# Kernel tuning notes

Hardware: AMD Instinct MI355X
Metric: run time of the kernel (lower is better)

Reference implementation:

```python
import jax, jax.numpy as jnp
import numpy as np

P = 8        # num policies
Z = 64       # per-policy latent dim
D = P * Z    # total latent dim = 512
A = 8        # action dim
H = 512      # hidden dim
B = 8192     # batch


def setup_inputs() -> dict:
    key = jax.random.key(0)
    ks = jax.random.split(key, 10)
    IN = Z + A
    s1 = 1.0 / np.sqrt(IN)
    s2 = 1.0 / np.sqrt(H)
    return {
        "latents": jax.random.normal(ks[0], (B, D), dtype=jnp.float32),
        "actions": jax.random.normal(ks[1], (B, A), dtype=jnp.float32),
        "policy_indices": jax.random.randint(ks[2], (B,), 0, P, dtype=jnp.int64) if jax.config.jax_enable_x64 else jax.random.randint(ks[2], (B,), 0, P, dtype=jnp.int32),
        # Stacked params for P_outer x P_inner MLPs: (z+A) -> H -> H -> Z
        "W1": jax.random.uniform(ks[3], (P, P, IN, H), jnp.float32, -s1, s1),
        "b1": jax.random.uniform(ks[4], (P, P, H), jnp.float32, -s1, s1),
        "W2": jax.random.uniform(ks[5], (P, P, H, H), jnp.float32, -s2, s2),
        "b2": jax.random.uniform(ks[6], (P, P, H), jnp.float32, -s2, s2),
        "W3": jax.random.uniform(ks[7], (P, P, H, Z), jnp.float32, -s2, s2),
        "b3": jax.random.uniform(ks[8], (P, P, Z), jnp.float32, -s2, s2),
    }


def reference(latents, actions, policy_indices, W1, b1, W2, b2, W3, b3):
    Bb, Dd = latents.shape
    Pp = W1.shape[0]
    Zz = Dd // Pp
    # split latent into per-policy chunks: [B, P, Z]
    pl = latents.reshape(Bb, Pp, Zz)
    # each inner MLP sees (its latent chunk, shared action): [B, P, Z+A]
    act = jnp.broadcast_to(actions[:, None, :], (Bb, Pp, actions.shape[-1]))
    x = jnp.concatenate([pl, act], axis=-1)
    out = jnp.zeros_like(latents)
    # loop over outer policy models (fixed small set); select rows by policy index
    for i in range(Pp):
        h = jax.nn.relu(jnp.einsum("bpi,pih->bph", x, W1[i]) + b1[i])
        h = jax.nn.relu(jnp.einsum("bph,phk->bpk", h, W2[i]) + b2[i])
        y = jnp.einsum("bph,phz->bpz", h, W3[i]) + b3[i]  # [B, P, Z]
        y = y.reshape(Bb, Dd)  # concat over inner policies
        out = jnp.where((policy_indices == i)[:, None], y, out)
    return out
```

## Files before the change

kernel.cpp:

```cpp
#include <hip/hip_runtime.h>
#include <stdint.h>

#define PNUM  8
#define DDIM  512
#define ZDIM  64
#define ADIM  8
#define HDIM  512
#define BATCH 8192
#define KIN   72
#define NKS1  3
#define NKS2  16
#define NKS3  16
#define NT12  32
#define NT3   4
#define TM    32
#define PXP   104
#define PHP   520

typedef __attribute__((ext_vector_type(8))) __bf16 bf16x8;
typedef __attribute__((ext_vector_type(4))) float  f32x4;

#define WS_COUNTS_I 0
#define WS_OFFS_I   16
#define WS_CURS_I   32
#define WS_FLG_I    42
#define WS_PERM_I   64
#define WS_W1P_B    40960
#define WS_W2P_B    (WS_W1P_B + 64*NKS1*NT12*1024)
#define WS_W3P_B    (WS_W2P_B + 64*NKS2*NT12*1024)
#define WS_NEED_B   (WS_W3P_B + 64*NKS3*NT3*1024)

__device__ __forceinline__ float bf2f(ushort h){
  union { unsigned int u; float f; } v; v.u = ((unsigned int)h) << 16; return v.f;
}
__device__ __forceinline__ ushort f2bf(float f){
  union { float f; unsigned int u; } v; v.f = f;
  unsigned int u = v.u;
  return (ushort)((u + 0x7FFFu + ((u >> 16) & 1u)) >> 16);
}
__device__ __forceinline__ unsigned int pk2(ushort lo, ushort hi){
  return (unsigned int)lo | ((unsigned int)hi << 16);
}
__device__ __forceinline__ float ldf(const void* p, size_t i, int f32){
  return f32 ? ((const float*)p)[i] : bf2f(((const ushort*)p)[i]);
}
__device__ __forceinline__ int ldidx(const void* p, int t, int i64){
  return i64 ? (int)((const long long*)p)[t] : ((const int*)p)[t];
}
__device__ __forceinline__ float4 ldbias4(const void* b, size_t off, int f32){
  if (f32) return *(const float4*)((const float*)b + off);
  ushort4 q = *(const ushort4*)((const ushort*)b + off);
  float4 r; r.x = bf2f(q.x); r.y = bf2f(q.y); r.z = bf2f(q.z); r.w = bf2f(q.w);
  return r;
}

__global__ void k_detect(const unsigned int* __restrict__ lat,
                         const unsigned int* __restrict__ act,
                         const unsigned int* __restrict__ w1,
                         const unsigned int* __restrict__ bb1,
                         const unsigned int* __restrict__ w2,
                         const unsigned int* __restrict__ bb2,
                         const unsigned int* __restrict__ w3,
                         const unsigned int* __restrict__ bb3,
                         const unsigned int* __restrict__ idx,
                         int* __restrict__ wsi){
  int t = threadIdx.x >> 6, lane = threadIdx.x & 63;
  if (t > 8) return;
  if (t == 8){
    unsigned long long nz = __ballot(idx[2 * lane + 1] != 0u);
    if (lane == 0) wsi[WS_FLG_I + 8] = (nz == 0ull) ? 1 : 0;
    return;
  }
  const unsigned int* ptrs[8] = {lat, act, w1, bb1, w2, bb2, w3, bb3};
  unsigned int u = ptrs[t][lane];
  unsigned int e = (u >> 7) & 0xFFu;
  unsigned long long ib = __ballot(e >= 100u && e <= 150u);
  if (lane == 0) wsi[WS_FLG_I + t] = (__popcll(ib) < 40) ? 1 : 0;
}

__global__ void k_sort(const void* __restrict__ idx, int* __restrict__ wsi){
  __shared__ int hist[PNUM];
  __shared__ int cur[PNUM];
  const int tid = threadIdx.x;
  const int i64 = wsi[WS_FLG_I + 8];
  if (tid < PNUM) hist[tid] = 0;
  __syncthreads();
  int pol[8];
  #pragma unroll
  for (int c = 0; c < 8; c++){
    int t = c * 1024 + tid;
    pol[c] = ldidx(idx, t, i64);
    atomicAdd(&hist[pol[c]], 1);
  }
  __syncthreads();
  if (tid == 0){
    int off = 0;
    #pragma unroll
    for (int i = 0; i < PNUM; i++){
      int h = hist[i];
      wsi[WS_COUNTS_I + i] = h;
      wsi[WS_OFFS_I + i] = off;
      cur[i] = off;
      off += h;
    }
  }
  __syncthreads();
  #pragma unroll
  for (int c = 0; c < 8; c++){
    int t = c * 1024 + tid;
    int pos = atomicAdd(&cur[pol[c]], 1);
    wsi[WS_PERM_I + pos] = t;
  }
}

__global__ void k_pack(const void* __restrict__ src, ushort* __restrict__ dst,
                       int Ksrc, int nks, int ntiles, int N,
                       const int* __restrict__ wsi, int flg){
  __shared__ ushort T[32][66];
  const int ks = blockIdx.y, pair = blockIdx.z, nt0 = blockIdx.x * 4;
  const int f32 = wsi[WS_FLG_I + flg];
  const int w = threadIdx.x >> 6, lane = threadIdx.x & 63;
  #pragma unroll
  for (int kk = 0; kk < 8; kk++){
    int krow = w * 8 + kk;
    int k = ks * 32 + krow;
    int n = nt0 * 16 + lane;
    ushort v = 0;
    if (k < Ksrc) v = f2bf(ldf(src, ((size_t)pair * Ksrc + k) * N + n, f32));
    T[krow][lane] = v;
  }
  __syncthreads();
  const int lm = lane & 15, lq = lane >> 4;
  unsigned int vv[4];
  #pragma unroll
  for (int j = 0; j < 4; j++){
    ushort lo = T[lq * 8 + 2 * j    ][w * 16 + lm];
    ushort hi = T[lq * 8 + 2 * j + 1][w * 16 + lm];
    vv[j] = pk2(lo, hi);
  }
  uint4 val = make_uint4(vv[0], vv[1], vv[2], vv[3]);
  size_t f = (size_t)(pair * nks + ks) * ntiles + (nt0 + w);
  *(uint4*)(dst + f * 512 + (size_t)lane * 8) = val;
}

__global__ void __launch_bounds__(512, 4) k_mlp(
    const void* __restrict__ latents, const void* __restrict__ actions,
    const void* __restrict__ b1, const void* __restrict__ b2,
    const void* __restrict__ b3,
    const int* __restrict__ wsi,
    const ushort* __restrict__ w1p, const ushort* __restrict__ w2p,
    const ushort* __restrict__ w3p,
    void* __restrict__ out, int out_elems)
{
  __shared__ __align__(16) ushort Xb [TM * PXP];
  __shared__ __align__(16) ushort H1s[TM * PHP];
  __shared__ __align__(16) ushort H2s[TM * PHP];
  __shared__ int rowid[TM];

  const int io = blockIdx.x >> 3, p = blockIdx.x & 7, tile = blockIdx.y;
  const int cnt = wsi[WS_COUNTS_I + io];
  if (tile * TM >= cnt) return;
  const int r0    = wsi[WS_OFFS_I + io] + tile * TM;
  const int mrows = min(TM, cnt - tile * TM);
  const int pair  = io * PNUM + p;
  const int tid   = threadIdx.x;
  const int fLat  = wsi[WS_FLG_I + 0];
  const int fAct  = wsi[WS_FLG_I + 1];
  const int fB1   = wsi[WS_FLG_I + 3];
  const int fB2   = wsi[WS_FLG_I + 5];
  const int fB3   = wsi[WS_FLG_I + 7];

  const int w = tid >> 6, lane = tid & 63;
  const int lm = lane & 15, lq = lane >> 4;
  const int ntb = w * 4;
  const uint4* w1v = (const uint4*)w1p;
  const uint4* w2v = (const uint4*)w2p;
  const uint4* w3v = (const uint4*)w3p;
  const f32x4 zero4 = {0.f, 0.f, 0.f, 0.f};

  uint4 a1w[NKS1][4];
  #pragma unroll
  for (int ks = 0; ks < NKS1; ks++)
    #pragma unroll
    for (int a = 0; a < 4; a++)
      a1w[ks][a] = w1v[((size_t)(pair * NKS1 + ks) * NT12 + ntb + a) * 64 + lane];

  for (int task = tid; task < TM * 16; task += 512){
    int r = task >> 4, c = task & 15;
    if (c >= 13) continue;
    uint4 val = make_uint4(0u, 0u, 0u, 0u);
    if (r < mrows){
      int row = wsi[WS_PERM_I + r0 + r];
      if (c == 8) rowid[r] = row;
      if (c < 9){
        int f32 = (c < 8) ? fLat : fAct;
        if (f32){
          const float* sf = (c < 8)
            ? ((const float*)latents + (size_t)row * DDIM + p * ZDIM + c * 8)
            : ((const float*)actions + (size_t)row * ADIM);
          float4 f0 = *(const float4*)sf;
          float4 f1 = *(const float4*)(sf + 4);
          val = make_uint4(pk2(f2bf(f0.x), f2bf(f0.y)),
                           pk2(f2bf(f0.z), f2bf(f0.w)),
                           pk2(f2bf(f1.x), f2bf(f1.y)),
                           pk2(f2bf(f1.z), f2bf(f1.w)));
        } else {
          const ushort* sh = (c < 8)
            ? ((const ushort*)latents + (size_t)row * DDIM + p * ZDIM + c * 8)
            : ((const ushort*)actions + (size_t)row * ADIM);
          val = *(const uint4*)sh;
        }
      }
    } else if (c == 8) rowid[r] = 0;
    *(uint4*)(Xb + r * PXP + c * 8) = val;
  }
  __syncthreads();

  #define MFMA8(A, B) \
    { _Pragma("unroll") for (int a_ = 0; a_ < 4; a_++) \
      { _Pragma("unroll") for (int m_ = 0; m_ < 2; m_++) \
        acc[a_][m_] = __builtin_amdgcn_mfma_f32_16x16x32_bf16( \
            __builtin_bit_cast(bf16x8, A[a_]), __builtin_bit_cast(bf16x8, B[m_]), \
            acc[a_][m_], 0, 0, 0); } }
  #define LDA2(dst, kss) \
    { _Pragma("unroll") for (int a_ = 0; a_ < 4; a_++) \
        dst[a_] = w2v[((size_t)(pair * NKS2 + (kss)) * NT12 + ntb + a_) * 64 + lane]; }
  #define LDB2(dst, kss) \
    { _Pragma("unroll") for (int m_ = 0; m_ < 2; m_++) \
        dst[m_] = *(const uint4*)(H1s + (size_t)(m_ * 16 + lm) * PHP + (kss) * 32 + lq * 8); }
  #define CP4(dst, srcv) \
    { _Pragma("unroll") for (int a_ = 0; a_ < 4; a_++) dst[a_] = srcv[a_]; }

  {
    f32x4 acc[4][2];
    #pragma unroll
    for (int a = 0; a < 4; a++)
      #pragma unroll
      for (int m = 0; m < 2; m++) acc[a][m] = zero4;

    #pragma unroll
    for (int ks = 0; ks < NKS1; ks++){
      uint4 bfm[2];
      #pragma unroll
      for (int m = 0; m < 2; m++)
        bfm[m] = *(const uint4*)(Xb + (size_t)(m * 16 + lm) * PXP + ks * 32 + lq * 8);
      MFMA8(a1w[ks], bfm);
    }
    #pragma unroll
    for (int a = 0; a < 4; a++){
      int n0 = (ntb + a) * 16 + lq * 4;
      float4 bq = ldbias4(b1, (size_t)pair * HDIM + n0, fB1);
      #pragma unroll
      for (int m = 0; m < 2; m++){
        ushort4 o;
        o.x = f2bf(fmaxf(acc[a][m][0] + bq.x, 0.f));
        o.y = f2bf(fmaxf(acc[a][m][1] + bq.y, 0.f));
        o.z = f2bf(fmaxf(acc[a][m][2] + bq.z, 0.f));
        o.w = f2bf(fmaxf(acc[a][m][3] + bq.w, 0.f));
        *(ushort4*)(H1s + (size_t)(m * 16 + lm) * PHP + n0) = o;
      }
    }
  }

  uint4 A0[4], A1[4];
  LDA2(A0, 0);
  LDA2(A1, 1);
  __syncthreads();

  {
    f32x4 acc[4][2];
    #pragma unroll
    for (int a = 0; a < 4; a++)
      #pragma unroll
      for (int m = 0; m < 2; m++) acc[a][m] = zero4;

    uint4 B0[2], B1[2];
    LDB2(B0, 0);
    #pragma unroll
    for (int ks = 0; ks < NKS2; ks += 2){
      uint4 TA[4];
      if (ks + 2 < NKS2) LDA2(TA, ks + 2);
      LDB2(B1, ks + 1);
      MFMA8(A0, B0);
      if (ks + 2 < NKS2) CP4(A0, TA);
      uint4 TB[4];
      if (ks + 3 < NKS2) LDA2(TB, ks + 3);
      if (ks + 2 < NKS2) LDB2(B0, ks + 2);
      MFMA8(A1, B1);
      if (ks + 3 < NKS2) CP4(A1, TB);
    }
    #pragma unroll
    for (int a = 0; a < 4; a++){
      int n0 = (ntb + a) * 16 + lq * 4;
      float4 bq = ldbias4(b2, (size_t)pair * HDIM + n0, fB2);
      #pragma unroll
      for (int m = 0; m < 2; m++){
        ushort4 o;
        o.x = f2bf(fmaxf(acc[a][m][0] + bq.x, 0.f));
        o.y = f2bf(fmaxf(acc[a][m][1] + bq.y, 0.f));
        o.z = f2bf(fmaxf(acc[a][m][2] + bq.z, 0.f));
        o.w = f2bf(fmaxf(acc[a][m][3] + bq.w, 0.f));
        *(ushort4*)(H2s + (size_t)(m * 16 + lm) * PHP + n0) = o;
      }
    }
  }

  const int zt = w & 3, mh = w >> 2;
  uint4 C0 = w3v[((size_t)(pair * NKS3 + 0) * NT3 + zt) * 64 + lane];
  uint4 C1 = w3v[((size_t)(pair * NKS3 + 1) * NT3 + zt) * 64 + lane];
  __syncthreads();

  {
    f32x4 acc3 = zero4;
    #pragma unroll
    for (int ks = 0; ks < NKS3; ks += 2){
      uint4 T0;
      if (ks + 2 < NKS3)
        T0 = w3v[((size_t)(pair * NKS3 + ks + 2) * NT3 + zt) * 64 + lane];
      uint4 bf = *(const uint4*)(H2s + (size_t)(mh * 16 + lm) * PHP + ks * 32 + lq * 8);
      acc3 = __builtin_amdgcn_mfma_f32_16x16x32_bf16(
          __builtin_bit_cast(bf16x8, C0), __builtin_bit_cast(bf16x8, bf), acc3, 0, 0, 0);
      if (ks + 2 < NKS3) C0 = T0;
      uint4 T1;
      if (ks + 3 < NKS3)
        T1 = w3v[((size_t)(pair * NKS3 + ks + 3) * NT3 + zt) * 64 + lane];
      uint4 bf2 = *(const uint4*)(H2s + (size_t)(mh * 16 + lm) * PHP + (ks + 1) * 32 + lq * 8);
      acc3 = __builtin_amdgcn_mfma_f32_16x16x32_bf16(
          __builtin_bit_cast(bf16x8, C1), __builtin_bit_cast(bf16x8, bf2), acc3, 0, 0, 0);
      if (ks + 3 < NKS3) C1 = T1;
    }
    int z0 = zt * 16 + lq * 4;
    float4 bq = ldbias4(b3, (size_t)pair * ZDIM + z0, fB3);
    int mm = mh * 16 + lm;
    if (mm < mrows){
      int row = rowid[mm];
      size_t oidx = (size_t)row * DDIM + p * ZDIM + z0;
      if (oidx + 4 <= (size_t)out_elems){
        if (fLat){
          float4 o;
          o.x = acc3[0] + bq.x;
          o.y = acc3[1] + bq.y;
          o.z = acc3[2] + bq.z;
          o.w = acc3[3] + bq.w;
          *(float4*)((float*)out + oidx) = o;
        } else {
          ushort4 o;
          o.x = f2bf(acc3[0] + bq.x);
          o.y = f2bf(acc3[1] + bq.y);
          o.z = f2bf(acc3[2] + bq.z);
          o.w = f2bf(acc3[3] + bq.w);
          *(ushort4*)((ushort*)out + oidx) = o;
        }
      }
    }
  }
  #undef MFMA8
  #undef LDA2
  #undef LDB2
  #undef CP4
}

extern "C" void kernel_launch(void* const* d_in, const int* in_sizes, int n_in,
                              void* d_out, int out_size, void* d_ws, size_t ws_size,
                              hipStream_t stream){
  if (n_in < 9) return;
  const void* latents = d_in[0];
  const void* actions = d_in[1];
  const void* pidx    = d_in[2];
  const void* W1      = d_in[3];
  const void* b1      = d_in[4];
  const void* W2      = d_in[5];
  const void* b2      = d_in[6];
  const void* W3      = d_in[7];
  const void* b3      = d_in[8];

  if (ws_size < (size_t)WS_NEED_B) return;

  int*    wsi = (int*)d_ws;
  char*   wsb = (char*)d_ws;
  ushort* w1p = (ushort*)(wsb + WS_W1P_B);
  ushort* w2p = (ushort*)(wsb + WS_W2P_B);
  ushort* w3p = (ushort*)(wsb + WS_W3P_B);

  k_detect <<<1, 576, 0, stream>>>(
      (const unsigned int*)latents, (const unsigned int*)actions,
      (const unsigned int*)W1, (const unsigned int*)b1,
      (const unsigned int*)W2, (const unsigned int*)b2,
      (const unsigned int*)W3, (const unsigned int*)b3,
      (const unsigned int*)pidx, wsi);
  k_sort   <<<1, 1024, 0, stream>>>(pidx, wsi);
  k_pack<<<dim3(8, NKS1, 64), 256, 0, stream>>>(W1, w1p, KIN,  NKS1, NT12, HDIM, wsi, 2);
  k_pack<<<dim3(8, NKS2, 64), 256, 0, stream>>>(W2, w2p, HDIM, NKS2, NT12, HDIM, wsi, 4);
  k_pack<<<dim3(1, NKS3, 64), 256, 0, stream>>>(W3, w3p, HDIM, NKS3, NT3,  ZDIM, wsi, 6);
  k_mlp<<<dim3(64, BATCH/TM), 512, 0, stream>>>(
      latents, actions, b1, b2, b3, wsi, w1p, w2p, w3p, d_out, out_size);
}
```

Measured before the change: 259.2 us.

## Double MLP row tile, merge prep and pack kernels, vectorize weight packing

Doubles the per-block row tile from 32 to 64 so each block's loaded weights serve more MFMA work, and lowers the launch-bounds occupancy hint to make room for the larger accumulator set. Bias loads are hoisted ahead of the GEMM loops. The detect and sort kernels are merged into one, and the three weight-pack launches become a single vectorized pack kernel, cutting launch count and scalar global loads. The larger tile raises register and LDS pressure and halves the block count, which can reduce occupancy.

Result: faster. 219.3 us (-15.4%).

```diff
diff --git a/kernel.cpp b/kernel.cpp
--- a/kernel.cpp
+++ b/kernel.cpp
@@ -13,7 +13,7 @@
 #define NKS3  16
 #define NT12  32
 #define NT3   4
-#define TM    32
+#define TM    64
 #define PXP   104
 #define PHP   520
 
@@ -41,9 +41,6 @@
 __device__ __forceinline__ unsigned int pk2(ushort lo, ushort hi){
   return (unsigned int)lo | ((unsigned int)hi << 16);
 }
-__device__ __forceinline__ float ldf(const void* p, size_t i, int f32){
-  return f32 ? ((const float*)p)[i] : bf2f(((const ushort*)p)[i]);
-}
 __device__ __forceinline__ int ldidx(const void* p, int t, int i64){
   return i64 ? (int)((const long long*)p)[t] : ((const int*)p)[t];
 }
@@ -54,42 +51,38 @@
   return r;
 }
 
-__global__ void k_detect(const unsigned int* __restrict__ lat,
-                         const unsigned int* __restrict__ act,
-                         const unsigned int* __restrict__ w1,
-                         const unsigned int* __restrict__ bb1,
-                         const unsigned int* __restrict__ w2,
-                         const unsigned int* __restrict__ bb2,
-                         const unsigned int* __restrict__ w3,
-                         const unsigned int* __restrict__ bb3,
-                         const unsigned int* __restrict__ idx,
-                         int* __restrict__ wsi){
-  int t = threadIdx.x >> 6, lane = threadIdx.x & 63;
-  if (t > 8) return;
-  if (t == 8){
-    unsigned long long nz = __ballot(idx[2 * lane + 1] != 0u);
-    if (lane == 0) wsi[WS_FLG_I + 8] = (nz == 0ull) ? 1 : 0;
-    return;
-  }
-  const unsigned int* ptrs[8] = {lat, act, w1, bb1, w2, bb2, w3, bb3};
-  unsigned int u = ptrs[t][lane];
-  unsigned int e = (u >> 7) & 0xFFu;
-  unsigned long long ib = __ballot(e >= 100u && e <= 150u);
-  if (lane == 0) wsi[WS_FLG_I + t] = (__popcll(ib) < 40) ? 1 : 0;
-}
-
-__global__ void k_sort(const void* __restrict__ idx, int* __restrict__ wsi){
+__global__ void k_prep(const unsigned int* __restrict__ lat,
+                       const unsigned int* __restrict__ act,
+                       const unsigned int* __restrict__ w1,
+                       const unsigned int* __restrict__ bb1,
+                       const unsigned int* __restrict__ w2,
+                       const unsigned int* __restrict__ bb2,
+                       const unsigned int* __restrict__ w3,
+                       const unsigned int* __restrict__ bb3,
+                       const void* __restrict__ idx,
+                       int* __restrict__ wsi){
   __shared__ int hist[PNUM];
   __shared__ int cur[PNUM];
+  __shared__ int flg_i64;
   const int tid = threadIdx.x;
-  const int i64 = wsi[WS_FLG_I + 8];
   if (tid < PNUM) hist[tid] = 0;
-  __syncthreads();
+  const int t = tid >> 6, lane = tid & 63;
+  if (t == 8){
+    unsigned long long nz = __ballot(((const unsigned int*)idx)[2 * lane + 1] != 0u);
+    if (lane == 0){ int v = (nz == 0ull) ? 1 : 0; wsi[WS_FLG_I + 8] = v; flg_i64 = v; }
+  } else if (t < 8){
+    const unsigned int* ptrs[8] = {lat, act, w1, bb1, w2, bb2, w3, bb3};
+    unsigned int u = ptrs[t][lane];
+    unsigned int e = (u >> 7) & 0xFFu;
+    unsigned long long ib = __ballot(e >= 100u && e <= 150u);
+    if (lane == 0) wsi[WS_FLG_I + t] = (__popcll(ib) < 40) ? 1 : 0;
+  }
+  __syncthreads();
+  const int i64 = flg_i64;
   int pol[8];
   #pragma unroll
   for (int c = 0; c < 8; c++){
-    int t = c * 1024 + tid;
-    pol[c] = ldidx(idx, t, i64);
+    pol[c] = ldidx(idx, c * 1024 + tid, i64);
     atomicAdd(&hist[pol[c]], 1);
   }
   __syncthreads();
@@ -107,29 +100,62 @@
   __syncthreads();
   #pragma unroll
   for (int c = 0; c < 8; c++){
-    int t = c * 1024 + tid;
     int pos = atomicAdd(&cur[pol[c]], 1);
-    wsi[WS_PERM_I + pos] = t;
-  }
-}
-
-__global__ void k_pack(const void* __restrict__ src, ushort* __restrict__ dst,
-                       int Ksrc, int nks, int ntiles, int N,
-                       const int* __restrict__ wsi, int flg){
-  __shared__ ushort T[32][66];
-  const int ks = blockIdx.y, pair = blockIdx.z, nt0 = blockIdx.x * 4;
+    wsi[WS_PERM_I + pos] = c * 1024 + tid;
+  }
+}
+
+#define PK_W1_N  1536
+#define PK_W2_N  8192
+#define PK_W3_N  1024
+__global__ void k_pack_all(const void* __restrict__ W1, const void* __restrict__ W2,
+                           const void* __restrict__ W3,
+                           ushort* __restrict__ w1p, ushort* __restrict__ w2p,
+                           ushort* __restrict__ w3p,
+                           const int* __restrict__ wsi){
+  __shared__ ushort T[32][80];
+  int bid = blockIdx.x;
+  const void* src; ushort* dst;
+  int Ksrc, nks, ntiles, N, flg, ntg, ks, pair;
+  if (bid < PK_W1_N){
+    src = W1; dst = w1p; Ksrc = KIN;  nks = NKS1; ntiles = NT12; N = HDIM; flg = 2;
+    pair = bid / 24; int rem = bid % 24; ks = rem >> 3; ntg = rem & 7;
+  } else if (bid < PK_W1_N + PK_W2_N){
+    int local = bid - PK_W1_N;
+    src = W2; dst = w2p; Ksrc = HDIM; nks = NKS2; ntiles = NT12; N = HDIM; flg = 4;
+    pair = local / 128; int rem = local % 128; ks = rem >> 3; ntg = rem & 7;
+  } else {
+    int local = bid - PK_W1_N - PK_W2_N;
+    src = W3; dst = w3p; Ksrc = HDIM; nks = NKS3; ntiles = NT3;  N = ZDIM; flg = 6;
+    pair = local / 16; ks = local % 16; ntg = 0;
+  }
   const int f32 = wsi[WS_FLG_I + flg];
-  const int w = threadIdx.x >> 6, lane = threadIdx.x & 63;
-  #pragma unroll
-  for (int kk = 0; kk < 8; kk++){
-    int krow = w * 8 + kk;
-    int k = ks * 32 + krow;
-    int n = nt0 * 16 + lane;
-    ushort v = 0;
-    if (k < Ksrc) v = f2bf(ldf(src, ((size_t)pair * Ksrc + k) * N + n, f32));
-    T[krow][lane] = v;
-  }
-  __syncthreads();
+  const int tid = threadIdx.x;
+  const int nb = ntg * 64;
+
+  if (f32){
+    #pragma unroll
+    for (int it = 0; it < 2; it++){
+      int i = it * 256 + tid;
+      int k = i >> 4, nq = i & 15;
+      int kk = ks * 32 + k;
+      float4 v = make_float4(0.f, 0.f, 0.f, 0.f);
+      if (kk < Ksrc)
+        v = *(const float4*)((const float*)src + ((size_t)pair * Ksrc + kk) * N + nb + nq * 4);
+      ushort4 o; o.x = f2bf(v.x); o.y = f2bf(v.y); o.z = f2bf(v.z); o.w = f2bf(v.w);
+      *(ushort4*)&T[k][nq * 4] = o;
+    }
+  } else {
+    int k = tid >> 3, uq = tid & 7;
+    int kk = ks * 32 + k;
+    uint4 v = make_uint4(0u, 0u, 0u, 0u);
+    if (kk < Ksrc)
+      v = *(const uint4*)((const ushort*)src + ((size_t)pair * Ksrc + kk) * N + nb + uq * 8);
+    *(uint4*)&T[k][uq * 8] = v;
+  }
+  __syncthreads();
+
+  const int w = tid >> 6, lane = tid & 63;
   const int lm = lane & 15, lq = lane >> 4;
   unsigned int vv[4];
   #pragma unroll
@@ -139,11 +165,11 @@
     vv[j] = pk2(lo, hi);
   }
   uint4 val = make_uint4(vv[0], vv[1], vv[2], vv[3]);
-  size_t f = (size_t)(pair * nks + ks) * ntiles + (nt0 + w);
+  size_t f = (size_t)(pair * nks + ks) * ntiles + (ntg * 4 + w);
   *(uint4*)(dst + f * 512 + (size_t)lane * 8) = val;
 }
 
-__global__ void __launch_bounds__(512, 4) k_mlp(
+__global__ void __launch_bounds__(512, 2) k_mlp(
     const void* __restrict__ latents, const void* __restrict__ actions,
     const void* __restrict__ b1, const void* __restrict__ b2,
     const void* __restrict__ b3,
@@ -184,6 +210,10 @@
     #pragma unroll
     for (int a = 0; a < 4; a++)
       a1w[ks][a] = w1v[((size_t)(pair * NKS1 + ks) * NT12 + ntb + a) * 64 + lane];
+  float4 bq1[4];
+  #pragma unroll
+  for (int a = 0; a < 4; a++)
+    bq1[a] = ldbias4(b1, (size_t)pair * HDIM + (ntb + a) * 16 + lq * 4, fB1);
 
   for (int task = tid; task < TM * 16; task += 512){
     int r = task >> 4, c = task & 15;
@@ -216,47 +246,46 @@
   }
   __syncthreads();
 
-  #define MFMA8(A, B) \
+  #define MFMA16(A, B) \
     { _Pragma("unroll") for (int a_ = 0; a_ < 4; a_++) \
-      { _Pragma("unroll") for (int m_ = 0; m_ < 2; m_++) \
+      { _Pragma("unroll") for (int m_ = 0; m_ < 4; m_++) \
         acc[a_][m_] = __builtin_amdgcn_mfma_f32_16x16x32_bf16( \
             __builtin_bit_cast(bf16x8, A[a_]), __builtin_bit_cast(bf16x8, B[m_]), \
             acc[a_][m_], 0, 0, 0); } }
   #define LDA2(dst, kss) \
     { _Pragma("unroll") for (int a_ = 0; a_ < 4; a_++) \
         dst[a_] = w2v[((size_t)(pair * NKS2 + (kss)) * NT12 + ntb + a_) * 64 + lane]; }
-  #define LDB2(dst, kss) \
-    { _Pragma("unroll") for (int m_ = 0; m_ < 2; m_++) \
+  #define LDB4(dst, kss) \
+    { _Pragma("unroll") for (int m_ = 0; m_ < 4; m_++) \
         dst[m_] = *(const uint4*)(H1s + (size_t)(m_ * 16 + lm) * PHP + (kss) * 32 + lq * 8); }
   #define CP4(dst, srcv) \
     { _Pragma("unroll") for (int a_ = 0; a_ < 4; a_++) dst[a_] = srcv[a_]; }
 
   {
-    f32x4 acc[4][2];
+    f32x4 acc[4][4];
     #pragma unroll
     for (int a = 0; a < 4; a++)
       #pragma unroll
-      for (int m = 0; m < 2; m++) acc[a][m] = zero4;
+      for (int m = 0; m < 4; m++) acc[a][m] = zero4;
 
     #pragma unroll
     for (int ks = 0; ks < NKS1; ks++){
-      uint4 bfm[2];
-      #pragma unroll
-      for (int m = 0; m < 2; m++)
+      uint4 bfm[4];
+      #pragma unroll
+      for (int m = 0; m < 4; m++)
         bfm[m] = *(const uint4*)(Xb + (size_t)(m * 16 + lm) * PXP + ks * 32 + lq * 8);
-      MFMA8(a1w[ks], bfm);
+      MFMA16(a1w[ks], bfm);
     }
     #pragma unroll
     for (int a = 0; a < 4; a++){
       int n0 = (ntb + a) * 16 + lq * 4;
-      float4 bq = ldbias4(b1, (size_t)pair * HDIM + n0, fB1);
-      #pragma unroll
-      for (int m = 0; m < 2; m++){
+      #pragma unroll
+      for (int m = 0; m < 4; m++){
         ushort4 o;
-        o.x = f2bf(fmaxf(acc[a][m][0] + bq.x, 0.f));
-        o.y = f2bf(fmaxf(acc[a][m][1] + bq.y, 0.f));
-        o.z = f2bf(fmaxf(acc[a][m][2] + bq.z, 0.f));
-        o.w = f2bf(fmaxf(acc[a][m][3] + bq.w, 0.f));
+        o.x = f2bf(fmaxf(acc[a][m][0] + bq1[a].x, 0.f));
+        o.y = f2bf(fmaxf(acc[a][m][1] + bq1[a].y, 0.f));
+        o.z = f2bf(fmaxf(acc[a][m][2] + bq1[a].z, 0.f));
+        o.w = f2bf(fmaxf(acc[a][m][3] + bq1[a].w, 0.f));
         *(ushort4*)(H1s + (size_t)(m * 16 + lm) * PHP + n0) = o;
       }
     }
@@ -265,98 +294,112 @@
   uint4 A0[4], A1[4];
   LDA2(A0, 0);
   LDA2(A1, 1);
+  float4 bq2[4];
+  #pragma unroll
+  for (int a = 0; a < 4; a++)
+    bq2[a] = ldbias4(b2, (size_t)pair * HDIM + (ntb + a) * 16 + lq * 4, fB2);
   __syncthreads();
 
   {
-    f32x4 acc[4][2];
+    f32x4 acc[4][4];
     #pragma unroll
     for (int a = 0; a < 4; a++)
       #pragma unroll
-      for (int m = 0; m < 2; m++) acc[a][m] = zero4;
-
-    uint4 B0[2], B1[2];
-    LDB2(B0, 0);
+      for (int m = 0; m < 4; m++) acc[a][m] = zero4;
+
+    uint4 B0[4], B1[4];
+    LDB4(B0, 0);
     #pragma unroll
     for (int ks = 0; ks < NKS2; ks += 2){
       uint4 TA[4];
       if (ks + 2 < NKS2) LDA2(TA, ks + 2);
-      LDB2(B1, ks + 1);
-      MFMA8(A0, B0);
+      LDB4(B1, ks + 1);
+      MFMA16(A0, B0);
       if (ks + 2 < NKS2) CP4(A0, TA);
       uint4 TB[4];
       if (ks + 3 < NKS2) LDA2(TB, ks + 3);
-      if (ks + 2 < NKS2) LDB2(B0, ks + 2);
-      MFMA8(A1, B1);
+      if (ks + 2 < NKS2) LDB4(B0, ks + 2);
+      MFMA16(A1, B1);
       if (ks + 3 < NKS2) CP4(A1, TB);
     }
     #pragma unroll
     for (int a = 0; a < 4; a++){
       int n0 = (ntb + a) * 16 + lq * 4;
-      float4 bq = ldbias4(b2, (size_t)pair * HDIM + n0, fB2);
-      #pragma unroll
-      for (int m = 0; m < 2; m++){
+      #pragma unroll
+      for (int m = 0; m < 4; m++){
         ushort4 o;
-        o.x = f2bf(fmaxf(acc[a][m][0] + bq.x, 0.f));
-        o.y = f2bf(fmaxf(acc[a][m][1] + bq.y, 0.f));
-        o.z = f2bf(fmaxf(acc[a][m][2] + bq.z, 0.f));
-        o.w = f2bf(fmaxf(acc[a][m][3] + bq.w, 0.f));
+        o.x = f2bf(fmaxf(acc[a][m][0] + bq2[a].x, 0.f));
+        o.y = f2bf(fmaxf(acc[a][m][1] + bq2[a].y, 0.f));
+        o.z = f2bf(fmaxf(acc[a][m][2] + bq2[a].z, 0.f));
+        o.w = f2bf(fmaxf(acc[a][m][3] + bq2[a].w, 0.f));
         *(ushort4*)(H2s + (size_t)(m * 16 + lm) * PHP + n0) = o;
       }
     }
   }
 
-  const int zt = w & 3, mh = w >> 2;
+  const int zt = w & 3, mb = w >> 2;
   uint4 C0 = w3v[((size_t)(pair * NKS3 + 0) * NT3 + zt) * 64 + lane];
   uint4 C1 = w3v[((size_t)(pair * NKS3 + 1) * NT3 + zt) * 64 + lane];
+  float4 bq3 = ldbias4(b3, (size_t)pair * ZDIM + zt * 16 + lq * 4, fB3);
   __syncthreads();
 
   {
-    f32x4 acc3 = zero4;
+    f32x4 acc3[2];
+    acc3[0] = zero4; acc3[1] = zero4;
     #pragma unroll
     for (int ks = 0; ks < NKS3; ks += 2){
-      uint4 T0;
+      uint4 T0, T1;
       if (ks + 2 < NKS3)
         T0 = w3v[((size_t)(pair * NKS3 + ks + 2) * NT3 + zt) * 64 + lane];
-      uint4 bf = *(const uint4*)(H2s + (size_t)(mh * 16 + lm) * PHP + ks * 32 + lq * 8);
-      acc3 = __builtin_amdgcn_mfma_f32_16x16x32_bf16(
-          __builtin_bit_cast(bf16x8, C0), __builtin_bit_cast(bf16x8, bf), acc3, 0, 0, 0);
-      if (ks + 2 < NKS3) C0 = T0;
-      uint4 T1;
       if (ks + 3 < NKS3)
         T1 = w3v[((size_t)(pair * NKS3 + ks + 3) * NT3 + zt) * 64 + lane];
-      uint4 bf2 = *(const uint4*)(H2s + (size_t)(mh * 16 + lm) * PHP + (ks + 1) * 32 + lq * 8);
-      acc3 = __builtin_amdgcn_mfma_f32_16x16x32_bf16(
-          __builtin_bit_cast(bf16x8, C1), __builtin_bit_cast(bf16x8, bf2), acc3, 0, 0, 0);
+      #pragma unroll
+      for (int h = 0; h < 2; h++){
+        int row = (mb + 2 * h) * 16 + lm;
+        uint4 bf = *(const uint4*)(H2s + (size_t)row * PHP + ks * 32 + lq * 8);
+        acc3[h] = __builtin_amdgcn_mfma_f32_16x16x32_bf16(
+            __builtin_bit_cast(bf16x8, C0), __builtin_bit_cast(bf16x8, bf), acc3[h], 0, 0, 0);
+      }
+      #pragma unroll
+      for (int h = 0; h < 2; h++){
+        int row = (mb + 2 * h) * 16 + lm;
+        uint4 bf = *(const uint4*)(H2s + (size_t)row * PHP + (ks + 1) * 32 + lq * 8);
+        acc3[h] = __builtin_amdgcn_mfma_f32_16x16x32_bf16(
+            __builtin_bit_cast(bf16x8, C1), __builtin_bit_cast(bf16x8, bf), acc3[h], 0, 0, 0);
+      }
+      if (ks + 2 < NKS3) C0 = T0;
       if (ks + 3 < NKS3) C1 = T1;
     }
     int z0 = zt * 16 + lq * 4;
-    float4 bq = ldbias4(b3, (size_t)pair * ZDIM + z0, fB3);
-    int mm = mh * 16 + lm;
-    if (mm < mrows){
-      int row = rowid[mm];
-      size_t oidx = (size_t)row * DDIM + p * ZDIM + z0;
-      if (oidx + 4 <= (size_t)out_elems){
-        if (fLat){
-          float4 o;
-          o.x = acc3[0] + bq.x;
-          o.y = acc3[1] + bq.y;
-          o.z = acc3[2] + bq.z;
-          o.w = acc3[3] + bq.w;
-          *(float4*)((float*)out + oidx) = o;
-        } else {
-          ushort4 o;
-          o.x = f2bf(acc3[0] + bq.x);
-          o.y = f2bf(acc3[1] + bq.y);
-          o.z = f2bf(acc3[2] + bq.z);
-          o.w = f2bf(acc3[3] + bq.w);
-          *(ushort4*)((ushort*)out + oidx) = o;
+    #pragma unroll
+    for (int h = 0; h < 2; h++){
+      int mm = (mb + 2 * h) * 16 + lm;
+      if (mm < mrows){
+        int row = rowid[mm];
+        size_t oidx = (size_t)row * DDIM + p * ZDIM + z0;
+        if (oidx + 4 <= (size_t)out_elems){
+          if (fLat){
+            float4 o;
+            o.x = acc3[h][0] + bq3.x;
+            o.y = acc3[h][1] + bq3.y;
+            o.z = acc3[h][2] + bq3.z;
+            o.w = acc3[h][3] + bq3.w;
+            *(float4*)((float*)out + oidx) = o;
+          } else {
+            ushort4 o;
+            o.x = f2bf(acc3[h][0] + bq3.x);
+            o.y = f2bf(acc3[h][1] + bq3.y);
+            o.z = f2bf(acc3[h][2] + bq3.z);
+            o.w = f2bf(acc3[h][3] + bq3.w);
+            *(ushort4*)((ushort*)out + oidx) = o;
+          }
         }
       }
     }
   }
-  #undef MFMA8
+  #undef MFMA16
   #undef LDA2
-  #undef LDB2
+  #undef LDB4
   #undef CP4
 }
 
@@ -382,16 +425,14 @@
   ushort* w2p = (ushort*)(wsb + WS_W2P_B);
   ushort* w3p = (ushort*)(wsb + WS_W3P_B);
 
-  k_detect <<<1, 576, 0, stream>>>(
+  k_prep<<<1, 1024, 0, stream>>>(
       (const unsigned int*)latents, (const unsigned int*)actions,
       (const unsigned int*)W1, (const unsigned int*)b1,
       (const unsigned int*)W2, (const unsigned int*)b2,
       (const unsigned int*)W3, (const unsigned int*)b3,
-      (const unsigned int*)pidx, wsi);
-  k_sort   <<<1, 1024, 0, stream>>>(pidx, wsi);
-  k_pack<<<dim3(8, NKS1, 64), 256, 0, stream>>>(W1, w1p, KIN,  NKS1, NT12, HDIM, wsi, 2);
-  k_pack<<<dim3(8, NKS2, 64), 256, 0, stream>>>(W2, w2p, HDIM, NKS2, NT12, HDIM, wsi, 4);
-  k_pack<<<dim3(1, NKS3, 64), 256, 0, stream>>>(W3, w3p, HDIM, NKS3, NT3,  ZDIM, wsi, 6);
+      pidx, wsi);
+  k_pack_all<<<PK_W1_N + PK_W2_N + PK_W3_N, 256, 0, stream>>>(
+      W1, W2, W3, w1p, w2p, w3p, wsi);
   k_mlp<<<dim3(64, BATCH/TM), 512, 0, stream>>>(
       latents, actions, b1, b2, b3, wsi, w1p, w2p, w3p, d_out, out_size);
 }
```
